# Kernel tuning notes

Measured on AMD Instinct MI355X. Metric: run time of the kernel, lower is better.

Reference implementation:

```python
import jax, jax.numpy as jnp
import numpy as np

N0, N1, N2, B = 1500000, 200000, 20000, 4096


def sage_conv(x_src, x_dst, src, dst, Wl, Wr, b, n_dst):
    # mean-aggregate neighbor features onto targets, then two linears + bias
    msg = x_src[src]                                             # [E, d]
    agg = jax.ops.segment_sum(msg, dst, num_segments=n_dst)       # [n_dst, d]
    cnt = jax.ops.segment_sum(jnp.ones(src.shape[0], x_src.dtype), dst, num_segments=n_dst)
    mean = agg / jnp.maximum(cnt, 1.0)[:, None]
    return mean @ Wl + x_dst @ Wr + b


def setup_inputs() -> dict:
    key = jax.random.key(0)
    ks = jax.random.split(key, 16)
    d_in, d_h, d_out = 100, 256, 47
    s = lambda k, sh, fan: jax.random.normal(k, sh, jnp.float32) * (1.0 / np.sqrt(fan))
    return {
        "x": jax.random.normal(ks[0], (N0, d_in), jnp.float32),
        "src0": jax.random.randint(ks[1], (2000000,), 0, N0),
        "dst0": jax.random.randint(ks[2], (2000000,), 0, N1),
        "src1": jax.random.randint(ks[3], (200000,), 0, N1),
        "dst1": jax.random.randint(ks[4], (200000,), 0, N2),
        "src2": jax.random.randint(ks[5], (20480,), 0, N2),
        "dst2": jax.random.randint(ks[6], (20480,), 0, B),
        "Wl0": s(ks[7], (d_in, d_h), d_in),
        "Wr0": s(ks[8], (d_in, d_h), d_in),
        "b0": jnp.zeros((d_h,), jnp.float32),
        "Wl1": s(ks[9], (d_h, d_h), d_h),
        "Wr1": s(ks[10], (d_h, d_h), d_h),
        "b1": jnp.zeros((d_h,), jnp.float32),
        "Wl2": s(ks[11], (d_h, d_out), d_h),
        "Wr2": s(ks[12], (d_h, d_out), d_h),
        "b2": jnp.zeros((d_out,), jnp.float32),
    }


def reference(x, src0, dst0, src1, dst1, src2, dst2,
              Wl0, Wr0, b0, Wl1, Wr1, b1, Wl2, Wr2, b2):
    # layer 0: sources = all sampled nodes, targets = first N1 nodes
    h = sage_conv(x, x[:N1], src0, dst0, Wl0, Wr0, b0, N1)
    h = jax.nn.relu(h)  # dropout is identity in eval mode
    # layer 1
    h = sage_conv(h, h[:N2], src1, dst1, Wl1, Wr1, b1, N2)
    h = jax.nn.relu(h)
    # layer 2 (final)
    h = sage_conv(h, h[:B], src2, dst2, Wl2, Wr2, b2, B)
    return jax.nn.log_softmax(h, axis=-1)
```

## Files before the change

kernel.cpp:

```cpp
#include <hip/hip_runtime.h>
#include <hip/hip_bf16.h>

#define N0   1500000
#define N1   200000
#define N2   20000
#define NB   4096
#define D_IN 100
#define D_H  256
#define D_OUT 47

#define K0P  224
#define K12P 512

#define SCAN_BLOCKS 256

typedef __bf16 bf16x8 __attribute__((ext_vector_type(8)));
typedef __bf16 bf16x4 __attribute__((ext_vector_type(4)));
typedef float  f32x4  __attribute__((ext_vector_type(4)));

__global__ void hist_kernel(const int* __restrict__ dst, int* __restrict__ deg, int E)
{
    int i = blockIdx.x * blockDim.x + threadIdx.x;
    if (i < E) atomicAdd(&deg[dst[i]], 1);
}

__global__ __launch_bounds__(256)
void scan_partial(const int* __restrict__ deg, int* __restrict__ partials, int n)
{
    const int b = blockIdx.x;
    const int chunk = (n + gridDim.x - 1) / gridDim.x;
    const int begin = b * chunk;
    const int end = min(begin + chunk, n);

    int s = 0;
    for (int i = begin + threadIdx.x; i < end; i += blockDim.x) s += deg[i];

    #pragma unroll
    for (int o = 32; o > 0; o >>= 1) s += __shfl_down(s, o);
    __shared__ int wsum[4];
    if ((threadIdx.x & 63) == 0) wsum[threadIdx.x >> 6] = s;
    __syncthreads();
    if (threadIdx.x == 0)
        partials[b] = wsum[0] + wsum[1] + wsum[2] + wsum[3];
}

__global__ __launch_bounds__(256)
void scan_offsets(int* __restrict__ partials, int* __restrict__ rowstart, int n)
{
    __shared__ int sm[256];
    const int t = threadIdx.x;
    sm[t] = partials[t];
    __syncthreads();
    for (int d = 1; d < 256; d <<= 1) {
        int val = sm[t];
        int oth = (t >= d) ? sm[t - d] : 0;
        __syncthreads();
        sm[t] = val + oth;
        __syncthreads();
    }
    partials[t] = (t > 0) ? sm[t - 1] : 0;
    if (t == 0) rowstart[n] = sm[255];
}

__global__ __launch_bounds__(256)
void scan_apply(const int* __restrict__ deg, const int* __restrict__ offsets,
                int* __restrict__ rowstart, int n)
{
    const int b = blockIdx.x;
    const int chunk = (n + gridDim.x - 1) / gridDim.x;
    const int begin = b * chunk;
    const int end = min(begin + chunk, n);

    __shared__ int sm[256];
    const int sub = (chunk + blockDim.x - 1) / blockDim.x;
    const int tb = begin + threadIdx.x * sub;
    const int te = min(tb + sub, end);

    int s = 0;
    for (int i = tb; i < te; ++i) s += deg[i];
    sm[threadIdx.x] = s;
    __syncthreads();
    for (int d = 1; d < 256; d <<= 1) {
        int val = sm[threadIdx.x];
        int oth = (threadIdx.x >= d) ? sm[threadIdx.x - d] : 0;
        __syncthreads();
        sm[threadIdx.x] = val + oth;
        __syncthreads();
    }
    int run = offsets[b] + ((threadIdx.x > 0) ? sm[threadIdx.x - 1] : 0);
    for (int i = tb; i < te; ++i) { rowstart[i] = run; run += deg[i]; }
}

__global__ void scatter_kernel(const int* __restrict__ src,
                               const int* __restrict__ dst,
                               const int* __restrict__ rowstart,
                               int* __restrict__ cursor,
                               int* __restrict__ csr_src, int E)
{
    int i = blockIdx.x * blockDim.x + threadIdx.x;
    if (i < E) {
        int t = dst[i];
        int pos = rowstart[t] + atomicAdd(&cursor[t], 1);
        csr_src[pos] = src[i];
    }
}

__global__ __launch_bounds__(256)
void gather_pack_l0(const float* __restrict__ x,
                    const int* __restrict__ rowstart,
                    const int* __restrict__ csr_src,
                    __bf16* __restrict__ A0, int nrows)
{
    const int wid  = (blockIdx.x * blockDim.x + threadIdx.x) >> 6;
    const int lane = threadIdx.x & 63;
    if (wid >= nrows) return;

    const int beg = rowstart[wid];
    const int end = rowstart[wid + 1];
    const bool act = lane < D_IN / 2;
    const int f = lane * 2;

    float s0 = 0, s1 = 0, t0 = 0, t1 = 0, u0 = 0, u1 = 0, v0 = 0, v1 = 0;
    int e = beg;
    for (; e + 4 <= end; e += 4) {
        int i0 = csr_src[e];
        int i1 = csr_src[e + 1];
        int i2 = csr_src[e + 2];
        int i3 = csr_src[e + 3];
        if (act) {
            float2 p0 = *reinterpret_cast<const float2*>(x + (long)i0 * D_IN + f);
            float2 p1 = *reinterpret_cast<const float2*>(x + (long)i1 * D_IN + f);
            float2 p2 = *reinterpret_cast<const float2*>(x + (long)i2 * D_IN + f);
            float2 p3 = *reinterpret_cast<const float2*>(x + (long)i3 * D_IN + f);
            s0 += p0.x; s1 += p0.y;
            t0 += p1.x; t1 += p1.y;
            u0 += p2.x; u1 += p2.y;
            v0 += p3.x; v1 += p3.y;
        }
    }
    for (; e < end; ++e) {
        int i0 = csr_src[e];
        if (act) {
            float2 p = *reinterpret_cast<const float2*>(x + (long)i0 * D_IN + f);
            s0 += p.x; s1 += p.y;
        }
    }

    const float inv = 1.0f / fmaxf((float)(end - beg), 1.0f);
    __bf16* o = A0 + (long)wid * K0P;
    const float* xd = x + (long)wid * D_IN;

    if (act) {
        float m0 = ((s0 + t0) + (u0 + v0)) * inv;
        float m1 = ((s1 + t1) + (u1 + v1)) * inv;
        o[f]     = (__bf16)m0;
        o[f + 1] = (__bf16)m1;
        float2 d = *reinterpret_cast<const float2*>(xd + f);
        o[D_IN + f]     = (__bf16)d.x;
        o[D_IN + f + 1] = (__bf16)d.y;
    }
    if (lane < K0P - 2 * D_IN) o[2 * D_IN + lane] = (__bf16)0.0f;
}

__global__ __launch_bounds__(256)
void gather_pack_h(const __bf16* __restrict__ h,
                   const int* __restrict__ rowstart,
                   const int* __restrict__ csr_src,
                   __bf16* __restrict__ Ap, int nrows)
{
    const int wid  = (blockIdx.x * blockDim.x + threadIdx.x) >> 6;
    const int lane = threadIdx.x & 63;
    if (wid >= nrows) return;

    const int beg = rowstart[wid];
    const int end = rowstart[wid + 1];

    float a[4] = {}, b[4] = {}, c[4] = {}, d[4] = {};
    int e = beg;
    for (; e + 4 <= end; e += 4) {
        int i0 = csr_src[e];
        int i1 = csr_src[e + 1];
        int i2 = csr_src[e + 2];
        int i3 = csr_src[e + 3];
        bf16x4 v0 = *reinterpret_cast<const bf16x4*>(h + (long)i0 * D_H + lane * 4);
        bf16x4 v1 = *reinterpret_cast<const bf16x4*>(h + (long)i1 * D_H + lane * 4);
        bf16x4 v2 = *reinterpret_cast<const bf16x4*>(h + (long)i2 * D_H + lane * 4);
        bf16x4 v3 = *reinterpret_cast<const bf16x4*>(h + (long)i3 * D_H + lane * 4);
        #pragma unroll
        for (int j = 0; j < 4; ++j) {
            a[j] += (float)v0[j]; b[j] += (float)v1[j];
            c[j] += (float)v2[j]; d[j] += (float)v3[j];
        }
    }
    for (; e < end; ++e) {
        bf16x4 v = *reinterpret_cast<const bf16x4*>(h + (long)csr_src[e] * D_H + lane * 4);
        #pragma unroll
        for (int j = 0; j < 4; ++j) a[j] += (float)v[j];
    }

    const float inv = 1.0f / fmaxf((float)(end - beg), 1.0f);
    bf16x4 m;
    #pragma unroll
    for (int j = 0; j < 4; ++j)
        m[j] = (__bf16)(((a[j] + b[j]) + (c[j] + d[j])) * inv);
    *reinterpret_cast<bf16x4*>(Ap + (long)wid * K12P + lane * 4) = m;

    bf16x4 own = *reinterpret_cast<const bf16x4*>(h + (long)wid * D_H + lane * 4);
    *reinterpret_cast<bf16x4*>(Ap + (long)wid * K12P + D_H + lane * 4) = own;
}

__global__ void pack_weights(const float* __restrict__ Wl,
                             const float* __restrict__ Wr,
                             __bf16* __restrict__ Wp,
                             int K1, int N, int Kpad)
{
    int n = blockIdx.x;
    for (int k = threadIdx.x; k < Kpad; k += blockDim.x) {
        float v = 0.0f;
        if (n < N) {
            if (k < K1)            v = Wl[(long)k * N + n];
            else if (k < 2 * K1)   v = Wr[(long)(k - K1) * N + n];
        }
        Wp[(long)n * Kpad + k] = (__bf16)v;
    }
}

#define BM 128
#define BK 32
#define LDK 40

template <int BN_T, int NT>
__global__ __launch_bounds__(NT)
void mfma_gemm(const __bf16* __restrict__ A,
               const __bf16* __restrict__ Bt,
               const float* __restrict__ bias,
               __bf16* __restrict__ Cbf,
               float* __restrict__ Cf,
               int M, int K, int Nreal, int relu)
{
    constexpr int WC = (NT / 64) / 2;
    static_assert(WC * 64 == BN_T, "wave grid must cover BN_T");
    constexpr int SIT = (BM + BN_T) * 4 / NT;

    __shared__ __bf16 As[BM * LDK];
    __shared__ __bf16 Bs[BN_T * LDK];

    const int tid  = threadIdx.x;
    const int lane = tid & 63;
    const int wv   = tid >> 6;
    const int wr   = wv / WC;
    const int wc   = wv % WC;
    const long row0 = (long)blockIdx.x * BM;
    const int  col0 = blockIdx.y * BN_T;

    f32x4 acc[4][4] = {};

    for (int k0 = 0; k0 < K; k0 += BK) {
        __syncthreads();
        #pragma unroll
        for (int i = 0; i < SIT; ++i) {
            int c  = tid + i * NT;
            int r  = c >> 2;
            int ko = (c & 3) * 8;
            if (r < BM) {
                long gr = row0 + r;
                if (gr > M - 1) gr = M - 1;
                *reinterpret_cast<uint4*>(&As[r * LDK + ko]) =
                    *reinterpret_cast<const uint4*>(&A[gr * K + k0 + ko]);
            } else {
                int br = r - BM;
                *reinterpret_cast<uint4*>(&Bs[br * LDK + ko]) =
                    *reinterpret_cast<const uint4*>(&Bt[(long)(col0 + br) * K + k0 + ko]);
            }
        }
        __syncthreads();

        bf16x8 a[4], b[4];
        #pragma unroll
        for (int mi = 0; mi < 4; ++mi)
            a[mi] = *reinterpret_cast<const bf16x8*>(
                &As[(wr * 64 + mi * 16 + (lane & 15)) * LDK + (lane >> 4) * 8]);
        #pragma unroll
        for (int ni = 0; ni < 4; ++ni)
            b[ni] = *reinterpret_cast<const bf16x8*>(
                &Bs[(wc * 64 + ni * 16 + (lane & 15)) * LDK + (lane >> 4) * 8]);

        #pragma unroll
        for (int mi = 0; mi < 4; ++mi)
            #pragma unroll
            for (int ni = 0; ni < 4; ++ni)
                acc[mi][ni] = __builtin_amdgcn_mfma_f32_16x16x32_bf16(
                    a[mi], b[ni], acc[mi][ni], 0, 0, 0);
    }

    const int colBase = col0 + wc * 64;
    #pragma unroll
    for (int mi = 0; mi < 4; ++mi) {
        const long rowBase = row0 + wr * 64 + mi * 16 + (lane >> 4) * 4;
        #pragma unroll
        for (int j = 0; j < 4; ++j) {
            long r = rowBase + j;
            if (r >= M) continue;
            #pragma unroll
            for (int ni = 0; ni < 4; ++ni) {
                int cc = colBase + ni * 16 + (lane & 15);
                if (cc >= Nreal) continue;
                float v = acc[mi][ni][j] + bias[cc];
                if (relu) v = fmaxf(v, 0.0f);
                if (Cbf) Cbf[r * Nreal + cc] = (__bf16)v;
                else     Cf [r * Nreal + cc] = v;
            }
        }
    }
}

__global__ void log_softmax_kernel(const float* __restrict__ in,
                                   float* __restrict__ out,
                                   int rows, int cols)
{
    int wave = (blockIdx.x * blockDim.x + threadIdx.x) / 64;
    int lane = threadIdx.x % 64;
    if (wave >= rows) return;

    const float* r = in + (long)wave * cols;
    float v = (lane < cols) ? r[lane] : -INFINITY;

    float m = v;
    #pragma unroll
    for (int o = 32; o > 0; o >>= 1) m = fmaxf(m, __shfl_xor(m, o));

    float e = (lane < cols) ? __expf(v - m) : 0.0f;
    float s = e;
    #pragma unroll
    for (int o = 32; o > 0; o >>= 1) s += __shfl_xor(s, o);

    float ls = logf(s);
    if (lane < cols)
        out[(long)wave * cols + lane] = v - m - ls;
}

extern "C" void kernel_launch(void* const* d_in, const int* in_sizes, int n_in,
                              void* d_out, int out_size, void* d_ws, size_t ws_size,
                              hipStream_t stream)
{
    const float* x    = (const float*)d_in[0];
    const int*   src0 = (const int*)d_in[1];
    const int*   dst0 = (const int*)d_in[2];
    const int*   src1 = (const int*)d_in[3];
    const int*   dst1 = (const int*)d_in[4];
    const int*   src2 = (const int*)d_in[5];
    const int*   dst2 = (const int*)d_in[6];
    const float* Wl0  = (const float*)d_in[7];
    const float* Wr0  = (const float*)d_in[8];
    const float* b0   = (const float*)d_in[9];
    const float* Wl1  = (const float*)d_in[10];
    const float* Wr1  = (const float*)d_in[11];
    const float* b1   = (const float*)d_in[12];
    const float* Wl2  = (const float*)d_in[13];
    const float* Wr2  = (const float*)d_in[14];
    const float* b2   = (const float*)d_in[15];
    float* out = (float*)d_out;

    const int E0 = in_sizes[1];
    const int E1 = in_sizes[3];
    const int E2 = in_sizes[5];

    char* wp = (char*)d_ws;
    auto alloc = [&](size_t bytes) -> char* {
        char* p = wp; wp += (bytes + 255) & ~(size_t)255; return p;
    };
    __bf16* A0   = (__bf16*)alloc((size_t)N1 * K0P * 2);
    __bf16* h0   = (__bf16*)alloc((size_t)N1 * D_H * 2);
    __bf16* A1   = (__bf16*)alloc((size_t)N2 * K12P * 2);
    __bf16* h1   = (__bf16*)alloc((size_t)N2 * D_H * 2);
    __bf16* A2   = (__bf16*)alloc((size_t)NB * K12P * 2);
    float*  logits = (float*)alloc((size_t)NB * D_OUT * 4);
    __bf16* Wp0  = (__bf16*)alloc((size_t)256 * K0P * 2);
    __bf16* Wp1  = (__bf16*)alloc((size_t)256 * K12P * 2);
    __bf16* Wp2  = (__bf16*)alloc((size_t)128 * K12P * 2);
    int* deg      = (int*)alloc((size_t)N1 * 4);
    int* cursor   = (int*)alloc((size_t)N1 * 4);
    int* rowstart = (int*)alloc((size_t)(N1 + 1) * 4);
    int* partials = (int*)alloc((size_t)SCAN_BLOCKS * 4);
    int* csr_src  = (int*)alloc((size_t)E0 * 4);

    pack_weights<<<256, 256, 0, stream>>>(Wl0, Wr0, Wp0, D_IN, D_H, K0P);
    pack_weights<<<256, 256, 0, stream>>>(Wl1, Wr1, Wp1, D_H, D_H, K12P);
    pack_weights<<<128, 256, 0, stream>>>(Wl2, Wr2, Wp2, D_H, D_OUT, K12P);

    hipMemsetAsync(deg, 0, (size_t)N1 * 4, stream);
    hipMemsetAsync(cursor, 0, (size_t)N1 * 4, stream);
    hist_kernel<<<(E0 + 255) / 256, 256, 0, stream>>>(dst0, deg, E0);
    scan_partial<<<SCAN_BLOCKS, 256, 0, stream>>>(deg, partials, N1);
    scan_offsets<<<1, 256, 0, stream>>>(partials, rowstart, N1);
    scan_apply<<<SCAN_BLOCKS, 256, 0, stream>>>(deg, partials, rowstart, N1);
    scatter_kernel<<<(E0 + 255) / 256, 256, 0, stream>>>(src0, dst0, rowstart, cursor, csr_src, E0);
    gather_pack_l0<<<(N1 + 3) / 4, 256, 0, stream>>>(x, rowstart, csr_src, A0, N1);
    {
        dim3 grid((N1 + BM - 1) / BM, 1);
        mfma_gemm<256, 512><<<grid, 512, 0, stream>>>(A0, Wp0, b0, h0, nullptr,
                                                      N1, K0P, D_H, 1);
    }

    hipMemsetAsync(deg, 0, (size_t)N2 * 4, stream);
    hipMemsetAsync(cursor, 0, (size_t)N2 * 4, stream);
    hist_kernel<<<(E1 + 255) / 256, 256, 0, stream>>>(dst1, deg, E1);
    scan_partial<<<SCAN_BLOCKS, 256, 0, stream>>>(deg, partials, N2);
    scan_offsets<<<1, 256, 0, stream>>>(partials, rowstart, N2);
    scan_apply<<<SCAN_BLOCKS, 256, 0, stream>>>(deg, partials, rowstart, N2);
    scatter_kernel<<<(E1 + 255) / 256, 256, 0, stream>>>(src1, dst1, rowstart, cursor, csr_src, E1);
    gather_pack_h<<<(N2 + 3) / 4, 256, 0, stream>>>(h0, rowstart, csr_src, A1, N2);
    {
        dim3 grid((N2 + BM - 1) / BM, 2);
        mfma_gemm<128, 256><<<grid, 256, 0, stream>>>(A1, Wp1, b1, h1, nullptr,
                                                      N2, K12P, D_H, 1);
    }

    hipMemsetAsync(deg, 0, (size_t)NB * 4, stream);
    hipMemsetAsync(cursor, 0, (size_t)NB * 4, stream);
    hist_kernel<<<(E2 + 255) / 256, 256, 0, stream>>>(dst2, deg, E2);
    scan_partial<<<SCAN_BLOCKS, 256, 0, stream>>>(deg, partials, NB);
    scan_offsets<<<1, 256, 0, stream>>>(partials, rowstart, NB);
    scan_apply<<<SCAN_BLOCKS, 256, 0, stream>>>(deg, partials, rowstart, NB);
    scatter_kernel<<<(E2 + 255) / 256, 256, 0, stream>>>(src2, dst2, rowstart, cursor, csr_src, E2);
    gather_pack_h<<<(NB + 3) / 4, 256, 0, stream>>>(h1, rowstart, csr_src, A2, NB);
    {
        dim3 grid((NB + BM - 1) / BM, 1);
        mfma_gemm<128, 256><<<grid, 256, 0, stream>>>(A2, Wp2, b2, nullptr, logits,
                                                      NB, K12P, D_OUT, 0);
    }

    {
        int waves_per_block = 256 / 64;
        int blocks = (NB + waves_per_block - 1) / waves_per_block;
        log_softmax_kernel<<<blocks, 256, 0, stream>>>(logits, out, NB, D_OUT);
    }
}
```

Measured before the change: 658.7 us.

## Unroll gathers by eight, load GEMM tiles direct to LDS, merge weight packing

The neighbor-gather kernels for layers 0 and 1+ now issue eight independent row loads per iteration with eight accumulators, putting more memory requests in flight per wave. The GEMM staging replaces register-routed global-to-shared copies with global_load_lds direct-to-LDS transfers into one unpadded shared buffer. The three weight-packing launches are merged into one kernel launch. The unpadded LDS layout (stride 32 instead of 40) may add bank conflicts on the MFMA fragment reads, and the larger unroll raises register use.

```diff
diff --git a/kernel.cpp b/kernel.cpp
--- a/kernel.cpp
+++ b/kernel.cpp
@@ -120,29 +120,42 @@
     const bool act = lane < D_IN / 2;
     const int f = lane * 2;
 
-    float s0 = 0, s1 = 0, t0 = 0, t1 = 0, u0 = 0, u1 = 0, v0 = 0, v1 = 0;
+    float ax[8], ay[8];
+    #pragma unroll
+    for (int u = 0; u < 8; ++u) { ax[u] = 0.0f; ay[u] = 0.0f; }
+
     int e = beg;
+    for (; e + 8 <= end; e += 8) {
+        int idx[8];
+        #pragma unroll
+        for (int u = 0; u < 8; ++u) idx[u] = csr_src[e + u];
+        if (act) {
+            float2 p[8];
+            #pragma unroll
+            for (int u = 0; u < 8; ++u)
+                p[u] = *reinterpret_cast<const float2*>(x + (long)idx[u] * D_IN + f);
+            #pragma unroll
+            for (int u = 0; u < 8; ++u) { ax[u] += p[u].x; ay[u] += p[u].y; }
+        }
+    }
     for (; e + 4 <= end; e += 4) {
-        int i0 = csr_src[e];
-        int i1 = csr_src[e + 1];
-        int i2 = csr_src[e + 2];
-        int i3 = csr_src[e + 3];
+        int idx[4];
+        #pragma unroll
+        for (int u = 0; u < 4; ++u) idx[u] = csr_src[e + u];
         if (act) {
-            float2 p0 = *reinterpret_cast<const float2*>(x + (long)i0 * D_IN + f);
-            float2 p1 = *reinterpret_cast<const float2*>(x + (long)i1 * D_IN + f);
-            float2 p2 = *reinterpret_cast<const float2*>(x + (long)i2 * D_IN + f);
-            float2 p3 = *reinterpret_cast<const float2*>(x + (long)i3 * D_IN + f);
-            s0 += p0.x; s1 += p0.y;
-            t0 += p1.x; t1 += p1.y;
-            u0 += p2.x; u1 += p2.y;
-            v0 += p3.x; v1 += p3.y;
+            float2 p[4];
+            #pragma unroll
+            for (int u = 0; u < 4; ++u)
+                p[u] = *reinterpret_cast<const float2*>(x + (long)idx[u] * D_IN + f);
+            #pragma unroll
+            for (int u = 0; u < 4; ++u) { ax[u] += p[u].x; ay[u] += p[u].y; }
         }
     }
     for (; e < end; ++e) {
         int i0 = csr_src[e];
         if (act) {
             float2 p = *reinterpret_cast<const float2*>(x + (long)i0 * D_IN + f);
-            s0 += p.x; s1 += p.y;
+            ax[0] += p.x; ay[0] += p.y;
         }
     }
 
@@ -151,10 +164,10 @@
     const float* xd = x + (long)wid * D_IN;
 
     if (act) {
-        float m0 = ((s0 + t0) + (u0 + v0)) * inv;
-        float m1 = ((s1 + t1) + (u1 + v1)) * inv;
-        o[f]     = (__bf16)m0;
-        o[f + 1] = (__bf16)m1;
+        float sx = ((ax[0] + ax[1]) + (ax[2] + ax[3])) + ((ax[4] + ax[5]) + (ax[6] + ax[7]));
+        float sy = ((ay[0] + ay[1]) + (ay[2] + ay[3])) + ((ay[4] + ay[5]) + (ay[6] + ay[7]));
+        o[f]     = (__bf16)(sx * inv);
+        o[f + 1] = (__bf16)(sy * inv);
         float2 d = *reinterpret_cast<const float2*>(xd + f);
         o[D_IN + f]     = (__bf16)d.x;
         o[D_IN + f + 1] = (__bf16)d.y;
@@ -174,47 +187,72 @@
 
     const int beg = rowstart[wid];
     const int end = rowstart[wid + 1];
-
-    float a[4] = {}, b[4] = {}, c[4] = {}, d[4] = {};
+    const __bf16* hf = h + lane * 4;
+
+    float acc[8][4];
+    #pragma unroll
+    for (int u = 0; u < 8; ++u)
+        #pragma unroll
+        for (int k = 0; k < 4; ++k) acc[u][k] = 0.0f;
+
     int e = beg;
+    for (; e + 8 <= end; e += 8) {
+        int idx[8];
+        #pragma unroll
+        for (int u = 0; u < 8; ++u) idx[u] = csr_src[e + u];
+        bf16x4 v[8];
+        #pragma unroll
+        for (int u = 0; u < 8; ++u)
+            v[u] = *reinterpret_cast<const bf16x4*>(hf + (long)idx[u] * D_H);
+        #pragma unroll
+        for (int u = 0; u < 8; ++u)
+            #pragma unroll
+            for (int k = 0; k < 4; ++k) acc[u][k] += (float)v[u][k];
+    }
     for (; e + 4 <= end; e += 4) {
-        int i0 = csr_src[e];
-        int i1 = csr_src[e + 1];
-        int i2 = csr_src[e + 2];
-        int i3 = csr_src[e + 3];
-        bf16x4 v0 = *reinterpret_cast<const bf16x4*>(h + (long)i0 * D_H + lane * 4);
-        bf16x4 v1 = *reinterpret_cast<const bf16x4*>(h + (long)i1 * D_H + lane * 4);
-        bf16x4 v2 = *reinterpret_cast<const bf16x4*>(h + (long)i2 * D_H + lane * 4);
-        bf16x4 v3 = *reinterpret_cast<const bf16x4*>(h + (long)i3 * D_H + lane * 4);
-        #pragma unroll
-        for (int j = 0; j < 4; ++j) {
-            a[j] += (float)v0[j]; b[j] += (float)v1[j];
-            c[j] += (float)v2[j]; d[j] += (float)v3[j];
-        }
+        int idx[4];
+        #pragma unroll
+        for (int u = 0; u < 4; ++u) idx[u] = csr_src[e + u];
+        bf16x4 v[4];
+        #pragma unroll
+        for (int u = 0; u < 4; ++u)
+            v[u] = *reinterpret_cast<const bf16x4*>(hf + (long)idx[u] * D_H);
+        #pragma unroll
+        for (int u = 0; u < 4; ++u)
+            #pragma unroll
+            for (int k = 0; k < 4; ++k) acc[u][k] += (float)v[u][k];
     }
     for (; e < end; ++e) {
-        bf16x4 v = *reinterpret_cast<const bf16x4*>(h + (long)csr_src[e] * D_H + lane * 4);
-        #pragma unroll
-        for (int j = 0; j < 4; ++j) a[j] += (float)v[j];
+        bf16x4 v = *reinterpret_cast<const bf16x4*>(hf + (long)csr_src[e] * D_H);
+        #pragma unroll
+        for (int k = 0; k < 4; ++k) acc[0][k] += (float)v[k];
     }
 
     const float inv = 1.0f / fmaxf((float)(end - beg), 1.0f);
     bf16x4 m;
     #pragma unroll
-    for (int j = 0; j < 4; ++j)
-        m[j] = (__bf16)(((a[j] + b[j]) + (c[j] + d[j])) * inv);
+    for (int k = 0; k < 4; ++k) {
+        float s = ((acc[0][k] + acc[1][k]) + (acc[2][k] + acc[3][k]))
+                + ((acc[4][k] + acc[5][k]) + (acc[6][k] + acc[7][k]));
+        m[k] = (__bf16)(s * inv);
+    }
     *reinterpret_cast<bf16x4*>(Ap + (long)wid * K12P + lane * 4) = m;
 
     bf16x4 own = *reinterpret_cast<const bf16x4*>(h + (long)wid * D_H + lane * 4);
     *reinterpret_cast<bf16x4*>(Ap + (long)wid * K12P + D_H + lane * 4) = own;
 }
 
-__global__ void pack_weights(const float* __restrict__ Wl,
-                             const float* __restrict__ Wr,
-                             __bf16* __restrict__ Wp,
-                             int K1, int N, int Kpad)
-{
-    int n = blockIdx.x;
+__global__ void pack_weights_all(const float* __restrict__ Wl0, const float* __restrict__ Wr0, __bf16* __restrict__ Wp0,
+                                 const float* __restrict__ Wl1, const float* __restrict__ Wr1, __bf16* __restrict__ Wp1,
+                                 const float* __restrict__ Wl2, const float* __restrict__ Wr2, __bf16* __restrict__ Wp2)
+{
+    int b = blockIdx.x;
+    const float* Wl; const float* Wr; __bf16* Wp;
+    int K1, N, Kpad, n;
+    if (b < 256)      { Wl = Wl0; Wr = Wr0; Wp = Wp0; K1 = D_IN; N = D_H;   Kpad = K0P;  n = b; }
+    else if (b < 512) { Wl = Wl1; Wr = Wr1; Wp = Wp1; K1 = D_H;  N = D_H;   Kpad = K12P; n = b - 256; }
+    else              { Wl = Wl2; Wr = Wr2; Wp = Wp2; K1 = D_H;  N = D_OUT; Kpad = K12P; n = b - 512; }
+
     for (int k = threadIdx.x; k < Kpad; k += blockDim.x) {
         float v = 0.0f;
         if (n < N) {
@@ -227,7 +265,6 @@
 
 #define BM 128
 #define BK 32
-#define LDK 40
 
 template <int BN_T, int NT>
 __global__ __launch_bounds__(NT)
@@ -241,9 +278,9 @@
     constexpr int WC = (NT / 64) / 2;
     static_assert(WC * 64 == BN_T, "wave grid must cover BN_T");
     constexpr int SIT = (BM + BN_T) * 4 / NT;
-
-    __shared__ __bf16 As[BM * LDK];
-    __shared__ __bf16 Bs[BN_T * LDK];
+    static_assert((BM * 4) % 64 == 0, "A/B staging boundary must be wave-aligned");
+
+    __shared__ __bf16 S[(BM + BN_T) * BK];
 
     const int tid  = threadIdx.x;
     const int lane = tid & 63;
@@ -262,16 +299,19 @@
             int c  = tid + i * NT;
             int r  = c >> 2;
             int ko = (c & 3) * 8;
+            const __bf16* g;
             if (r < BM) {
                 long gr = row0 + r;
                 if (gr > M - 1) gr = M - 1;
-                *reinterpret_cast<uint4*>(&As[r * LDK + ko]) =
-                    *reinterpret_cast<const uint4*>(&A[gr * K + k0 + ko]);
+                g = &A[gr * K + k0 + ko];
             } else {
-                int br = r - BM;
-                *reinterpret_cast<uint4*>(&Bs[br * LDK + ko]) =
-                    *reinterpret_cast<const uint4*>(&Bt[(long)(col0 + br) * K + k0 + ko]);
+                g = &Bt[(long)(col0 + (r - BM)) * K + k0 + ko];
             }
+            __bf16* ldsb = &S[(size_t)(i * NT + wv * 64) * 8];
+            __builtin_amdgcn_global_load_lds(
+                (const __attribute__((address_space(1))) void*)g,
+                (__attribute__((address_space(3))) void*)ldsb,
+                16, 0, 0);
         }
         __syncthreads();
 
@@ -279,11 +319,11 @@
         #pragma unroll
         for (int mi = 0; mi < 4; ++mi)
             a[mi] = *reinterpret_cast<const bf16x8*>(
-                &As[(wr * 64 + mi * 16 + (lane & 15)) * LDK + (lane >> 4) * 8]);
+                &S[(wr * 64 + mi * 16 + (lane & 15)) * BK + (lane >> 4) * 8]);
         #pragma unroll
         for (int ni = 0; ni < 4; ++ni)
             b[ni] = *reinterpret_cast<const bf16x8*>(
-                &Bs[(wc * 64 + ni * 16 + (lane & 15)) * LDK + (lane >> 4) * 8]);
+                &S[(BM + wc * 64 + ni * 16 + (lane & 15)) * BK + (lane >> 4) * 8]);
 
         #pragma unroll
         for (int mi = 0; mi < 4; ++mi)
@@ -384,9 +424,7 @@
     int* partials = (int*)alloc((size_t)SCAN_BLOCKS * 4);
     int* csr_src  = (int*)alloc((size_t)E0 * 4);
 
-    pack_weights<<<256, 256, 0, stream>>>(Wl0, Wr0, Wp0, D_IN, D_H, K0P);
-    pack_weights<<<256, 256, 0, stream>>>(Wl1, Wr1, Wp1, D_H, D_H, K12P);
-    pack_weights<<<128, 256, 0, stream>>>(Wl2, Wr2, Wp2, D_H, D_OUT, K12P);
+    pack_weights_all<<<640, 256, 0, stream>>>(Wl0, Wr0, Wp0, Wl1, Wr1, Wp1, Wl2, Wr2, Wp2);
 
     hipMemsetAsync(deg, 0, (size_t)N1 * 4, stream);
     hipMemsetAsync(cursor, 0, (size_t)N1 * 4, stream);
```

Result: faster. 634.2 us (-3.7%).
